# Performance work log

Hardware: AMD Instinct MI355X
Metric: run time of the kernel (lower is better)

## Reference

```python
import math
import jax, jax.numpy as jnp
import numpy as np


def _precompute_psi(nlat_in, nlon_in, nlat_out, K, theta_cutoff):
    """Faithful numpy port of _precompute_convolution_tensor (equiangular grids).
    Returns COO indices (k, t, lat_in, lon_in) and float values of the sparse
    filter tensor psi of logical shape [K, nlat_out, nlat_in*nlon_in]."""
    lats_in = np.linspace(0.0, np.pi, nlat_in)
    lats_out = np.linspace(0.0, np.pi, nlat_out)
    phis = np.linspace(-np.pi, np.pi, nlon_in)
    d_theta = theta_cutoff / K
    theta_i = np.arange(K) * d_theta  # (K,)
    ks, ts, las, los, vs = [], [], [], [], []
    alpha = -lats_in[:, None]          # (nlat_in, 1)
    beta = phis[None, :]               # (1, nlon_in)
    for t in range(nlat_out):
        gamma = lats_out[t]
        z = np.cos(alpha) * np.cos(gamma) - np.cos(beta) * np.sin(alpha) * np.sin(gamma)
        theta = np.arccos(np.clip(z, -1.0, 1.0))   # (nlat_in, nlon_in)
        diff = np.abs(theta[None, :, :] - theta_i[:, None, None])  # (K, nlat_in, nlon_in)
        mask = (diff < d_theta) & (theta[None, :, :] < theta_cutoff)
        k_idx, la_idx, lo_idx = np.nonzero(mask)
        v = 1.0 - diff[k_idx, la_idx, lo_idx] / d_theta  # triangle (hat) weights
        ks.append(k_idx); ts.append(np.full_like(k_idx, t)); las.append(la_idx); los.append(lo_idx); vs.append(v)
    return (np.concatenate(ks).astype(np.int32),
            np.concatenate(ts).astype(np.int32),
            np.concatenate(las).astype(np.int32),
            np.concatenate(los).astype(np.int32),
            np.concatenate(vs).astype(np.float32))


def setup_inputs() -> dict:
    B, C = 4, 32
    nlat_in, nlon_in = 361, 720
    nlat_out, nlon_out = 361, 720
    K = 3
    theta_cutoff = 0.01 * math.pi  # default used at the precompute call site
    k, t, la, lo, v = _precompute_psi(nlat_in, nlon_in, nlat_out, K, theta_cutoff)
    key = jax.random.key(0)
    x = jax.random.normal(key, (B, C, nlat_in, nlon_in), dtype=jnp.float32)
    return {
        "x": x,
        "psi_vals": jnp.asarray(v),
        "psi_k": jnp.asarray(k),
        "psi_t": jnp.asarray(t),
        "psi_lat": jnp.asarray(la),
        "psi_lon": jnp.asarray(lo),
        "kernel_size": K,
        "nlat_out": nlat_out,
        "nlon_out": nlon_out,
    }


def reference(x, psi_vals, psi_k, psi_t, psi_lat, psi_lon, kernel_size, nlat_out, nlon_out):
    B, C, nlat_in, nlon_in = x.shape
    BC = B * C
    scale = nlon_in // nlon_out  # = 1 here
    # (nlat_in, nlon_in, BC) layout, matching x.reshape(B*C,...).permute(1,2,0)
    xr = x.reshape(BC, nlat_in, nlon_in).transpose(1, 2, 0)
    seg = psi_k * nlat_out + psi_t           # row id in the (K*nlat_out) output
    num_seg = kernel_size * nlat_out

    def step(_, p):
        # torch.roll(x, scale, dims=lon) applied (p+1) times before the bmm:
        # rolled[lat, lon] = x[lat, (lon - (p+1)*scale) % nlon]
        lon_idx = (psi_lon - (p + 1) * scale) % nlon_in
        g = xr[psi_lat, lon_idx]             # (nnz, BC) irregular gather
        out_p = jax.ops.segment_sum(psi_vals[:, None] * g, seg, num_segments=num_seg)
        return None, out_p                   # (K*nlat_out, BC)

    _, outs = jax.lax.scan(step, None, jnp.arange(nlon_out))  # (nlon_out, K*nlat_out, BC)
    outs = outs.reshape(nlon_out, kernel_size, nlat_out, BC)
    # permute(3,1,2,0) then split BC -> (B, C)
    return outs.transpose(3, 1, 2, 0).reshape(B, C, kernel_size, nlat_out, nlon_out)
```

## Files before the change

kernel.cpp:

```cpp
#include <hip/hip_runtime.h>
#include <math.h>


#define NLAT 361
#define NLON 720
#define KK 3
#define PTILE 48
#define NPX 15
#define NT 384
#define PD 56
#define SWN 832
#define TOTCAP (720*1024)

typedef __attribute__((ext_vector_type(8))) short bf16x8;
typedef __attribute__((ext_vector_type(4))) float f32x4;
typedef __attribute__((ext_vector_type(4))) unsigned int u32x4;

#define D_PI 3.14159265358979311599796346854418516159057617187500
#define STEP_LAT (D_PI / 360.0)
#define STEP_PHI ((2.0 * D_PI) / 719.0)
#define CUTOFF (0.01 * D_PI)
#define DTH (CUTOFF / 3.0)

__device__ __forceinline__ void gll16(const void* g, void* l) {
    __builtin_amdgcn_global_load_lds(
        (const __attribute__((address_space(1))) void*)g,
        (__attribute__((address_space(3))) void*)l, 16, 0, 0);
}
__device__ __forceinline__ void gll4(const void* g, void* l) {
    __builtin_amdgcn_global_load_lds(
        (const __attribute__((address_space(1))) void*)g,
        (__attribute__((address_space(3))) void*)l, 4, 0, 0);
}

__device__ inline unsigned int bf16pair_rne(float lo, float hi) {
    unsigned int a = __builtin_bit_cast(unsigned int, lo);
    unsigned int b = __builtin_bit_cast(unsigned int, hi);
    a = a + 0x7fffu + ((a >> 16) & 1u);
    b = b + 0x7fffu + ((b >> 16) & 1u);
    return (a >> 16) | (b & 0xffff0000u);
}

__global__ __launch_bounds__(512) void bounds_kernel(int4* __restrict__ params,
                                                     float2* __restrict__ pAB,
                                                     unsigned long long* __restrict__ actd) {
    __shared__ int part[512];
    int tid = threadIdx.x;
    int rmins[9], Ws[9], bl8s[9];
    float As[9], Bs[9];
    int wsum = 0;
    if (tid < NLAT) {
        int t = tid;
        double g = (t == 360) ? D_PI : (double)t * STEP_LAT;
        double cg = cos(g), sg = sin(g);
        const double coscut = cos(CUTOFF);
#pragma unroll
        for (int d = 0; d < 9; ++d) {
            int la = t + d - 4;
            int rmin = 0, W = 0;
            double A = 0.0, Bc = 0.0;
            if (la >= 0 && la <= 360) {
                double lad = (la == 360) ? D_PI : (double)la * STEP_LAT;
                A = cos(lad) * cg;
                Bc = sin(lad) * sg;
                if (Bc < 1e-14) {
                    if (A > coscut) { rmin = 0; W = 720; }
                } else {
                    double C = (coscut - A) / Bc;
                    if (C <= -1.0) { rmin = 0; W = 720; }
                    else if (C < 1.0) {
                        double bmax = acos(C);
                        int r0 = (int)floor((D_PI - bmax) / STEP_PHI) + 1;
                        int r1 = (int)ceil((D_PI + bmax) / STEP_PHI) - 1;
                        if (r0 < 0) r0 = 0;
                        if (r1 > 719) r1 = 719;
                        rmin = r0; W = r1 - r0 + 1;
                        if (W < 0) W = 0;
                    }
                }
            }
            rmins[d] = rmin; Ws[d] = W;
            As[d] = (float)A; Bs[d] = (float)Bc;
            int b8 = 0;
            if (W > 0) {
                b8 = (W + 111) & ~7;
                if (b8 > SWN) b8 = SWN;
            }
            bl8s[d] = b8;
            wsum += b8;
        }
    }
    part[tid] = wsum;
    __syncthreads();
    for (int dd = 1; dd < 512; dd <<= 1) {
        int v = part[tid];
        int w2 = (tid >= dd) ? part[tid - dd] : 0;
        __syncthreads();
        part[tid] = v + w2;
        __syncthreads();
    }
    int base = part[tid] - wsum;
    if (tid < NLAT) {
        unsigned long long pk = 0;
        int nact = 0;
#pragma unroll
        for (int d = 0; d < 9; ++d) {
            int off = base;
            base += bl8s[d];
            if (Ws[d] > 0 && off + bl8s[d] <= TOTCAP) {
                params[tid * 9 + d] = make_int4(rmins[d], Ws[d], off, bl8s[d]);
                pAB[tid * 9 + d] = make_float2(As[d], Bs[d]);
                pk |= ((unsigned long long)d) << (4 + 4 * nact);
                nact++;
            } else {
                params[tid * 9 + d] = make_int4(0, 0, 0, 0);
            }
        }
        pk |= (unsigned long long)nact;
        actd[tid] = pk;
    }
}

__global__ __launch_bounds__(128) void fill_w_kernel(const int4* __restrict__ params,
                                                     const float2* __restrict__ pAB,
                                                     unsigned int* __restrict__ wtab) {
    int row = blockIdx.x;
    int4 pr = params[row];
    int W = pr.y;
    if (W <= 0) return;
    int rmin = pr.x, off = pr.z, bl8 = pr.w;
    float2 ab = pAB[row];
    float A = ab.x, Bc = ab.y;
    const float invd = (float)(1.0 / DTH);
    for (int idx = threadIdx.x; idx < bl8; idx += 128) {
        int j = idx - PD;
        float f1 = 1.0e9f, f2 = 1.0e9f;
        if (j >= 0 && j < W) {
            int lo = rmin + j;
            float beta = (lo == 719) ? (float)D_PI : (float)((double)lo * STEP_PHI - D_PI);
            float z = fminf(1.f, fmaxf(-1.f, fmaf(Bc, cosf(beta), A)));
            f1 = acosf(z) * invd;
        }
        if (j + 1 >= 0 && j + 1 < W) {
            int lo = rmin + j + 1;
            float beta = (lo == 719) ? (float)D_PI : (float)((double)lo * STEP_PHI - D_PI);
            float z = fminf(1.f, fmaxf(-1.f, fmaf(Bc, cosf(beta), A)));
            f2 = acosf(z) * invd;
        }
        float w0a = fmaxf(0.f, 1.f - f1);
        float w1a = fmaxf(0.f, 1.f - fabsf(f1 - 1.f));
        float w2a = fmaxf(0.f, 1.f - fabsf(f1 - 2.f));
        float w0b = fmaxf(0.f, 1.f - f2);
        float w1b = fmaxf(0.f, 1.f - fabsf(f2 - 1.f));
        float w2b = fmaxf(0.f, 1.f - fabsf(f2 - 2.f));
        wtab[0 * TOTCAP + off + idx] = bf16pair_rne(w0a, w0b);
        wtab[1 * TOTCAP + off + idx] = bf16pair_rne(w1a, w1b);
        wtab[2 * TOTCAP + off + idx] = bf16pair_rne(w2a, w2b);
    }
}

__global__ void cvt_x_kernel(const float* __restrict__ x, unsigned int* __restrict__ xb,
                             int n8) {
    for (int i = blockIdx.x * 256 + threadIdx.x; i < n8; i += gridDim.x * 256) {
        f32x4 a = *(const f32x4*)(x + (size_t)i * 8);
        f32x4 b = *(const f32x4*)(x + (size_t)i * 8 + 4);
        u32x4 q;
        q.x = bf16pair_rne(a.x, a.y);
        q.y = bf16pair_rne(a.z, a.w);
        q.z = bf16pair_rne(b.x, b.y);
        q.w = bf16pair_rne(b.z, b.w);
        *(u32x4*)(xb + (size_t)i * 4) = q;
    }
}

template <int USEBF16>
__global__ __launch_bounds__(NT, 4) void dconv_mfma_kernel(
    const float* __restrict__ x, const unsigned short* __restrict__ xb,
    const int4* __restrict__ params, const unsigned long long* __restrict__ actd,
    const unsigned int* __restrict__ wtab, float* __restrict__ out) {
    __shared__ __attribute__((aligned(16))) unsigned char sB[2][128 * 128];
    __shared__ unsigned int sWi[2][KK * SWN];

    int bid = blockIdx.x;
    int r = bid & 7;
    int rest = bid >> 3;
    int px = rest % NPX;
    int q = rest / NPX;
    int yp = 8 * q + r;
    if (yp > 360) return;
    int t = (yp & 1) ? (360 - (yp >> 1)) : (yp >> 1);
    int p0 = px * PTILE;
    int tid = threadIdx.x;
    int lane = tid & 63;
    int w = tid >> 6;
    int psub = w >> 1;
    int bc0w = (w & 1) * 64;
    int l15 = lane & 15;
    int l4 = lane >> 4;

    f32x4 acc[4][KK];
#pragma unroll
    for (int n = 0; n < 4; ++n)
#pragma unroll
        for (int k = 0; k < KK; ++k) acc[n][k] = (f32x4){0.f, 0.f, 0.f, 0.f};

    unsigned long long pk = actd[t];
    int nact = (int)(pk & 15ull);

    int c = 0, iact = 0;
    int la = 0, W = 0, off = 0, bl8 = 0, mbase = 0, shift = 0;
    int nK = 0, nC = 1, ks_lo = 0, ks_hi = -1;

    auto LOADP = [&](int dd) {
        la = t + dd - 4;
        int4 pr = params[t * 9 + dd];
        int rmin = pr.x;
        W = pr.y; off = pr.z; bl8 = pr.w;
        int ms0 = rmin - 48 - p0;
        shift = (ms0 + 720) & 7;
        nK = (W + 47 + shift + 31) >> 5;
        nC = (nK + 1) >> 1;
        mbase = (((ms0 - shift) % 720) + 720) % 720;
        int s_off = psub * 16 + 9 - shift;
        int kl = (9 - s_off + 31) >> 5;
        ks_lo = kl < 0 ? 0 : kl;
        int kh = (55 + W - s_off) >> 5;
        ks_hi = kh > nK - 1 ? nK - 1 : kh;
    };

    auto ISSUE = [&](int cc, bool rowstart, int pbuf, int rbuf) {
#pragma unroll
        for (int pass = 0; pass < 3; ++pass) {
            int slot = pass * NT + tid;
            if (slot < 1024) {
                int bc = slot >> 3;
                int g = slot & 7;
                int gs = g ^ (bc & 7);
                int mg = mbase + cc * 64 + gs * 8;
                mg -= (mg >= 720) ? 720 : 0;
                mg -= (mg >= 720) ? 720 : 0;
                mg -= (mg >= 720) ? 720 : 0;
                if (USEBF16) {
                    gll16(xb + ((size_t)bc * NLAT + la) * NLON + mg,
                          &sB[pbuf][slot * 16]);
                } else {
                    const float* src = x + ((size_t)bc * NLAT + la) * NLON + mg;
                    f32x4 a = *(const f32x4*)(src);
                    f32x4 b = *(const f32x4*)(src + 4);
                    u32x4 qq;
                    qq.x = bf16pair_rne(a.x, a.y);
                    qq.y = bf16pair_rne(a.z, a.w);
                    qq.z = bf16pair_rne(b.x, b.y);
                    qq.w = bf16pair_rne(b.z, b.w);
                    *(u32x4*)(&sB[pbuf][slot * 16]) = qq;
                }
            }
        }
        if (rowstart) {
#pragma unroll
            for (int pass = 0; pass < 3; ++pass) {
                int idx = pass * NT + tid;
                if (idx < bl8) {
                    if (USEBF16) {
                        gll4(wtab + 0 * TOTCAP + off + idx, &sWi[rbuf][0 * SWN + idx]);
                        gll4(wtab + 1 * TOTCAP + off + idx, &sWi[rbuf][1 * SWN + idx]);
                        gll4(wtab + 2 * TOTCAP + off + idx, &sWi[rbuf][2 * SWN + idx]);
                    } else {
                        sWi[rbuf][0 * SWN + idx] = wtab[0 * TOTCAP + off + idx];
                        sWi[rbuf][1 * SWN + idx] = wtab[1 * TOTCAP + off + idx];
                        sWi[rbuf][2 * SWN + idx] = wtab[2 * TOTCAP + off + idx];
                    }
                }
            }
        }
    };

    LOADP((int)((pk >> 4) & 15ull));
    ISSUE(0, true, 0, 0);
    int pb = 0, rw = 0;

    while (true) {
        int shiftS = shift;
        int c2 = c * 2;
        int kloS = ks_lo > c2 ? ks_lo : c2;
        int khiS = ks_hi < c2 + 1 ? ks_hi : c2 + 1;
        int pbC = pb, rwC = rw;
        bool done = false, nrow = false;
        if (c + 1 < nC) {
            c = c + 1;
        } else if (iact + 1 < nact) {
            iact++;
            c = 0;
            LOADP((int)((pk >> (4 + 4 * iact)) & 15ull));
            nrow = true;
        } else {
            done = true;
        }
        if (USEBF16) asm volatile("s_waitcnt vmcnt(0)" ::: "memory");
        __syncthreads();
        if (!done) {
            pb ^= 1;
            if (nrow) rw ^= 1;
            ISSUE(c, nrow, pb, rw);
        }
        int soffS = psub * 16 + 9 - shiftS;
        for (int ks = kloS; ks <= khiS; ++ks) {
            int ksl = ks - c2;
            int s = ks * 32 + l4 * 8 + soffS + l15;
            bf16x8 af[KK];
#pragma unroll
            for (int k = 0; k < KK; ++k) {
                const unsigned int* wp = &sWi[rwC][k * SWN + s];
                u32x4 qf;
                qf.x = wp[0];
                qf.y = wp[2];
                qf.z = wp[4];
                qf.w = wp[6];
                af[k] = __builtin_bit_cast(bf16x8, qf);
            }
            int colbase = ksl * 64 + l4 * 16;
#pragma unroll
            for (int n = 0; n < 4; ++n) {
                int brow = bc0w + n * 16 + l15;
                int colb = colbase ^ ((brow & 7) << 4);
                bf16x8 bfv = *(const bf16x8*)(&sB[pbC][brow * 128 + colb]);
                acc[n][0] = __builtin_amdgcn_mfma_f32_16x16x32_bf16(af[0], bfv, acc[n][0], 0, 0, 0);
                acc[n][1] = __builtin_amdgcn_mfma_f32_16x16x32_bf16(af[1], bfv, acc[n][1], 0, 0, 0);
                acc[n][2] = __builtin_amdgcn_mfma_f32_16x16x32_bf16(af[2], bfv, acc[n][2], 0, 0, 0);
            }
        }
        if (done) break;
    }

    int p = p0 + psub * 16 + l4 * 4;
#pragma unroll
    for (int n = 0; n < 4; ++n) {
        int bc = bc0w + n * 16 + l15;
#pragma unroll
        for (int k = 0; k < KK; ++k) {
            float* o = out + (((size_t)bc * KK + k) * NLAT + t) * NLON + p;
            *(f32x4*)o = acc[n][k];
        }
    }
}

extern "C" void kernel_launch(void* const* d_in, const int* in_sizes, int n_in,
                              void* d_out, int out_size, void* d_ws, size_t ws_size,
                              hipStream_t stream) {
    const float* x = (const float*)d_in[0];
    float* out = (float*)d_out;

    char* ws = (char*)d_ws;
    int4* params = (int4*)(ws + 0);
    float2* pAB = (float2*)(ws + 53248);
    unsigned long long* actd = (unsigned long long*)(ws + 81920);
    unsigned int* wtab = (unsigned int*)(ws + 90112);
    size_t xb_off = (90112 + (size_t)3 * TOTCAP * 4 + 4095) & ~(size_t)4095;
    size_t xb_bytes = (size_t)128 * NLAT * NLON * 2;
    int use_bf16 = (ws_size >= xb_off + xb_bytes) ? 1 : 0;
    unsigned short* xb = (unsigned short*)(ws + xb_off);

    bounds_kernel<<<1, 512, 0, stream>>>(params, pAB, actd);
    fill_w_kernel<<<NLAT * 9, 128, 0, stream>>>(params, pAB, wtab);

    dim3 grid(8 * NPX * 46, 1, 1);
    if (use_bf16) {
        int n8 = 128 * NLAT * NLON / 8;
        cvt_x_kernel<<<2048, 256, 0, stream>>>(x, (unsigned int*)xb, n8);
        dconv_mfma_kernel<1><<<grid, NT, 0, stream>>>(x, xb, params, actd, wtab, out);
    } else {
        dconv_mfma_kernel<0><<<grid, NT, 0, stream>>>(x, xb, params, actd, wtab, out);
    }
}
```

Before: 292.4 us.

## Read filter weights directly from global memory instead of staging in LDS

The weight table is re-laid out so the three kernel-size weights for each position sit next to each other (interleaved by 3). The LDS staging buffer for weights and its per-row async loads are removed. Each wave now loads its A-fragments straight from global or L2 into registers before issuing the next B tile, and the inner k-step loop is unrolled into two fixed halves. This cuts LDS usage, which may raise occupancy, and removes the per-row weight copy. The cost is scattered, non-vectorised global loads that sit on the critical path after the barrier.

```diff
diff --git a/kernel.cpp b/kernel.cpp
--- a/kernel.cpp
+++ b/kernel.cpp
@@ -26,11 +26,6 @@
     __builtin_amdgcn_global_load_lds(
         (const __attribute__((address_space(1))) void*)g,
         (__attribute__((address_space(3))) void*)l, 16, 0, 0);
-}
-__device__ __forceinline__ void gll4(const void* g, void* l) {
-    __builtin_amdgcn_global_load_lds(
-        (const __attribute__((address_space(1))) void*)g,
-        (__attribute__((address_space(3))) void*)l, 4, 0, 0);
 }
 
 __device__ inline unsigned int bf16pair_rne(float lo, float hi) {
@@ -153,9 +148,10 @@
         float w0b = fmaxf(0.f, 1.f - f2);
         float w1b = fmaxf(0.f, 1.f - fabsf(f2 - 1.f));
         float w2b = fmaxf(0.f, 1.f - fabsf(f2 - 2.f));
-        wtab[0 * TOTCAP + off + idx] = bf16pair_rne(w0a, w0b);
-        wtab[1 * TOTCAP + off + idx] = bf16pair_rne(w1a, w1b);
-        wtab[2 * TOTCAP + off + idx] = bf16pair_rne(w2a, w2b);
+        size_t e = (size_t)(off + idx) * 3;
+        wtab[e + 0] = bf16pair_rne(w0a, w0b);
+        wtab[e + 1] = bf16pair_rne(w1a, w1b);
+        wtab[e + 2] = bf16pair_rne(w2a, w2b);
     }
 }
 
@@ -179,7 +175,6 @@
     const int4* __restrict__ params, const unsigned long long* __restrict__ actd,
     const unsigned int* __restrict__ wtab, float* __restrict__ out) {
     __shared__ __attribute__((aligned(16))) unsigned char sB[2][128 * 128];
-    __shared__ unsigned int sWi[2][KK * SWN];
 
     int bid = blockIdx.x;
     int r = bid & 7;
@@ -208,14 +203,14 @@
     int nact = (int)(pk & 15ull);
 
     int c = 0, iact = 0;
-    int la = 0, W = 0, off = 0, bl8 = 0, mbase = 0, shift = 0;
+    int la = 0, W = 0, off = 0, mbase = 0, shift = 0;
     int nK = 0, nC = 1, ks_lo = 0, ks_hi = -1;
 
     auto LOADP = [&](int dd) {
         la = t + dd - 4;
         int4 pr = params[t * 9 + dd];
         int rmin = pr.x;
-        W = pr.y; off = pr.z; bl8 = pr.w;
+        W = pr.y; off = pr.z;
         int ms0 = rmin - 48 - p0;
         shift = (ms0 + 720) & 7;
         nK = (W + 47 + shift + 31) >> 5;
@@ -228,7 +223,7 @@
         ks_hi = kh > nK - 1 ? nK - 1 : kh;
     };
 
-    auto ISSUE = [&](int cc, bool rowstart, int pbuf, int rbuf) {
+    auto ISSUE = [&](int cc, int pbuf) {
 #pragma unroll
         for (int pass = 0; pass < 3; ++pass) {
             int slot = pass * NT + tid;
@@ -256,69 +251,63 @@
                 }
             }
         }
-        if (rowstart) {
-#pragma unroll
-            for (int pass = 0; pass < 3; ++pass) {
-                int idx = pass * NT + tid;
-                if (idx < bl8) {
-                    if (USEBF16) {
-                        gll4(wtab + 0 * TOTCAP + off + idx, &sWi[rbuf][0 * SWN + idx]);
-                        gll4(wtab + 1 * TOTCAP + off + idx, &sWi[rbuf][1 * SWN + idx]);
-                        gll4(wtab + 2 * TOTCAP + off + idx, &sWi[rbuf][2 * SWN + idx]);
-                    } else {
-                        sWi[rbuf][0 * SWN + idx] = wtab[0 * TOTCAP + off + idx];
-                        sWi[rbuf][1 * SWN + idx] = wtab[1 * TOTCAP + off + idx];
-                        sWi[rbuf][2 * SWN + idx] = wtab[2 * TOTCAP + off + idx];
-                    }
-                }
-            }
-        }
     };
 
     LOADP((int)((pk >> 4) & 15ull));
-    ISSUE(0, true, 0, 0);
-    int pb = 0, rw = 0;
+    ISSUE(0, 0);
+    int pb = 0;
 
     while (true) {
-        int shiftS = shift;
         int c2 = c * 2;
-        int kloS = ks_lo > c2 ? ks_lo : c2;
-        int khiS = ks_hi < c2 + 1 ? ks_hi : c2 + 1;
-        int pbC = pb, rwC = rw;
-        bool done = false, nrow = false;
+        bool do0 = (c2 >= ks_lo) && (c2 <= ks_hi);
+        bool do1 = (c2 + 1 >= ks_lo) && (c2 + 1 <= ks_hi);
+        int soffS = psub * 16 + 9 - shift;
+        int offS = off;
+        int pbC = pb;
+        bool done = false;
         if (c + 1 < nC) {
             c = c + 1;
         } else if (iact + 1 < nact) {
             iact++;
             c = 0;
             LOADP((int)((pk >> (4 + 4 * iact)) & 15ull));
-            nrow = true;
         } else {
             done = true;
         }
         if (USEBF16) asm volatile("s_waitcnt vmcnt(0)" ::: "memory");
         __syncthreads();
+        unsigned int A0[KK][4], A1[KK][4];
+        if (do0) {
+            int s0 = c2 * 32 + l4 * 8 + soffS + l15;
+            const unsigned int* bp = wtab + (size_t)(offS + s0) * 3;
+#pragma unroll
+            for (int e = 0; e < 4; ++e)
+#pragma unroll
+                for (int k = 0; k < KK; ++k)
+                    A0[k][e] = bp[e * 6 + k];
+        }
+        if (do1) {
+            int s1 = (c2 + 1) * 32 + l4 * 8 + soffS + l15;
+            const unsigned int* bp = wtab + (size_t)(offS + s1) * 3;
+#pragma unroll
+            for (int e = 0; e < 4; ++e)
+#pragma unroll
+                for (int k = 0; k < KK; ++k)
+                    A1[k][e] = bp[e * 6 + k];
+        }
         if (!done) {
             pb ^= 1;
-            if (nrow) rw ^= 1;
-            ISSUE(c, nrow, pb, rw);
-        }
-        int soffS = psub * 16 + 9 - shiftS;
-        for (int ks = kloS; ks <= khiS; ++ks) {
-            int ksl = ks - c2;
-            int s = ks * 32 + l4 * 8 + soffS + l15;
+            ISSUE(c, pb);
+        }
+        if (do0) {
             bf16x8 af[KK];
 #pragma unroll
             for (int k = 0; k < KK; ++k) {
-                const unsigned int* wp = &sWi[rwC][k * SWN + s];
                 u32x4 qf;
-                qf.x = wp[0];
-                qf.y = wp[2];
-                qf.z = wp[4];
-                qf.w = wp[6];
+                qf.x = A0[k][0]; qf.y = A0[k][1]; qf.z = A0[k][2]; qf.w = A0[k][3];
                 af[k] = __builtin_bit_cast(bf16x8, qf);
             }
-            int colbase = ksl * 64 + l4 * 16;
+            int colbase = l4 * 16;
 #pragma unroll
             for (int n = 0; n < 4; ++n) {
                 int brow = bc0w + n * 16 + l15;
@@ -329,6 +318,25 @@
                 acc[n][2] = __builtin_amdgcn_mfma_f32_16x16x32_bf16(af[2], bfv, acc[n][2], 0, 0, 0);
             }
         }
+        if (do1) {
+            bf16x8 af[KK];
+#pragma unroll
+            for (int k = 0; k < KK; ++k) {
+                u32x4 qf;
+                qf.x = A1[k][0]; qf.y = A1[k][1]; qf.z = A1[k][2]; qf.w = A1[k][3];
+                af[k] = __builtin_bit_cast(bf16x8, qf);
+            }
+            int colbase = 64 + l4 * 16;
+#pragma unroll
+            for (int n = 0; n < 4; ++n) {
+                int brow = bc0w + n * 16 + l15;
+                int colb = colbase ^ ((brow & 7) << 4);
+                bf16x8 bfv = *(const bf16x8*)(&sB[pbC][brow * 128 + colb]);
+                acc[n][0] = __builtin_amdgcn_mfma_f32_16x16x32_bf16(af[0], bfv, acc[n][0], 0, 0, 0);
+                acc[n][1] = __builtin_amdgcn_mfma_f32_16x16x32_bf16(af[1], bfv, acc[n][1], 0, 0, 0);
+                acc[n][2] = __builtin_amdgcn_mfma_f32_16x16x32_bf16(af[2], bfv, acc[n][2], 0, 0, 0);
+            }
+        }
         if (done) break;
     }
 
@@ -355,7 +363,7 @@
     float2* pAB = (float2*)(ws + 53248);
     unsigned long long* actd = (unsigned long long*)(ws + 81920);
     unsigned int* wtab = (unsigned int*)(ws + 90112);
-    size_t xb_off = (90112 + (size_t)3 * TOTCAP * 4 + 4095) & ~(size_t)4095;
+    size_t xb_off = (90112 + (size_t)TOTCAP * 12 + 4095) & ~(size_t)4095;
     size_t xb_bytes = (size_t)128 * NLAT * NLON * 2;
     int use_bf16 = (ws_size >= xb_off + xb_bytes) ? 1 : 0;
     unsigned short* xb = (unsigned short*)(ws + xb_off);
```

Result: slower. 308.2 us (+5.4%).

## Double chunk width to 128 columns and stream weight slices per chunk

Applied to the files above, without the earlier changes.

Each pipeline stage now stages 128 longitude columns per bc row instead of 64, so there are half as many barrier-synchronised chunks. Filter weights are no longer loaded once per active latitude row into a large table. Instead a small 192-entry slice per plane is double-buffered alongside each B chunk. Shared memory per block grows to about 68 KB and launch bounds drop to 3 blocks per SM, trading occupancy for fewer syncs and a simpler weight-load path. The inner k-step loop is unrolled by 4 with guards.

```diff
diff --git a/kernel.cpp b/kernel.cpp
--- a/kernel.cpp
+++ b/kernel.cpp
@@ -10,7 +10,9 @@
 #define NT 384
 #define PD 56
 #define SWN 832
+#define SWNP 192
 #define TOTCAP (720*1024)
+#define BUFB (128*256)
 
 typedef __attribute__((ext_vector_type(8))) short bf16x8;
 typedef __attribute__((ext_vector_type(4))) float f32x4;
@@ -174,19 +176,19 @@
 }
 
 template <int USEBF16>
-__global__ __launch_bounds__(NT, 4) void dconv_mfma_kernel(
+__global__ __launch_bounds__(NT, 3) void dconv_mfma_kernel(
     const float* __restrict__ x, const unsigned short* __restrict__ xb,
     const int4* __restrict__ params, const unsigned long long* __restrict__ actd,
     const unsigned int* __restrict__ wtab, float* __restrict__ out) {
-    __shared__ __attribute__((aligned(16))) unsigned char sB[2][128 * 128];
-    __shared__ unsigned int sWi[2][KK * SWN];
+    __shared__ __attribute__((aligned(16))) unsigned char sB[2][BUFB];
+    __shared__ __attribute__((aligned(16))) unsigned int sWi[2][3 * SWNP];
 
     int bid = blockIdx.x;
     int r = bid & 7;
     int rest = bid >> 3;
     int px = rest % NPX;
-    int q = rest / NPX;
-    int yp = 8 * q + r;
+    int qg = rest / NPX;
+    int yp = 8 * qg + r;
     if (yp > 360) return;
     int t = (yp & 1) ? (360 - (yp >> 1)) : (yp >> 1);
     int p0 = px * PTILE;
@@ -208,18 +210,18 @@
     int nact = (int)(pk & 15ull);
 
     int c = 0, iact = 0;
-    int la = 0, W = 0, off = 0, bl8 = 0, mbase = 0, shift = 0;
+    int la = 0, W = 0, off = 0, mbase = 0, shift = 0;
     int nK = 0, nC = 1, ks_lo = 0, ks_hi = -1;
 
     auto LOADP = [&](int dd) {
         la = t + dd - 4;
         int4 pr = params[t * 9 + dd];
         int rmin = pr.x;
-        W = pr.y; off = pr.z; bl8 = pr.w;
+        W = pr.y; off = pr.z;
         int ms0 = rmin - 48 - p0;
         shift = (ms0 + 720) & 7;
         nK = (W + 47 + shift + 31) >> 5;
-        nC = (nK + 1) >> 1;
+        nC = (nK + 3) >> 2;
         mbase = (((ms0 - shift) % 720) + 720) % 720;
         int s_off = psub * 16 + 9 - shift;
         int kl = (9 - s_off + 31) >> 5;
@@ -228,15 +230,15 @@
         ks_hi = kh > nK - 1 ? nK - 1 : kh;
     };
 
-    auto ISSUE = [&](int cc, bool rowstart, int pbuf, int rbuf) {
-#pragma unroll
-        for (int pass = 0; pass < 3; ++pass) {
+    auto ISSUE = [&](int cc, int pbuf) {
+#pragma unroll
+        for (int pass = 0; pass < 6; ++pass) {
             int slot = pass * NT + tid;
-            if (slot < 1024) {
-                int bc = slot >> 3;
-                int g = slot & 7;
-                int gs = g ^ (bc & 7);
-                int mg = mbase + cc * 64 + gs * 8;
+            if (slot < 2048) {
+                int bc = slot >> 4;
+                int g = slot & 15;
+                int gs = (g & 8) | ((g ^ (bc & 7)) & 7);
+                int mg = mbase + cc * 128 + gs * 8;
                 mg -= (mg >= 720) ? 720 : 0;
                 mg -= (mg >= 720) ? 720 : 0;
                 mg -= (mg >= 720) ? 720 : 0;
@@ -256,43 +258,40 @@
                 }
             }
         }
-        if (rowstart) {
-#pragma unroll
-            for (int pass = 0; pass < 3; ++pass) {
-                int idx = pass * NT + tid;
-                if (idx < bl8) {
-                    if (USEBF16) {
-                        gll4(wtab + 0 * TOTCAP + off + idx, &sWi[rbuf][0 * SWN + idx]);
-                        gll4(wtab + 1 * TOTCAP + off + idx, &sWi[rbuf][1 * SWN + idx]);
-                        gll4(wtab + 2 * TOTCAP + off + idx, &sWi[rbuf][2 * SWN + idx]);
-                    } else {
-                        sWi[rbuf][0 * SWN + idx] = wtab[0 * TOTCAP + off + idx];
-                        sWi[rbuf][1 * SWN + idx] = wtab[1 * TOTCAP + off + idx];
-                        sWi[rbuf][2 * SWN + idx] = wtab[2 * TOTCAP + off + idx];
-                    }
+#pragma unroll
+        for (int pass = 0; pass < 2; ++pass) {
+            int slot = pass * NT + tid;
+            if (slot < 3 * SWNP) {
+                int plane = slot / SWNP;
+                int e = slot - plane * SWNP;
+                int gidx = off + cc * 128 + e;
+                gidx = (gidx > TOTCAP - 1) ? (TOTCAP - 1) : gidx;
+                if (USEBF16) {
+                    gll4(wtab + (size_t)plane * TOTCAP + gidx, &sWi[pbuf][slot]);
+                } else {
+                    sWi[pbuf][slot] = wtab[(size_t)plane * TOTCAP + gidx];
                 }
             }
         }
     };
 
     LOADP((int)((pk >> 4) & 15ull));
-    ISSUE(0, true, 0, 0);
-    int pb = 0, rw = 0;
+    ISSUE(0, 0);
+    int pb = 0;
 
     while (true) {
-        int shiftS = shift;
-        int c2 = c * 2;
-        int kloS = ks_lo > c2 ? ks_lo : c2;
-        int khiS = ks_hi < c2 + 1 ? ks_hi : c2 + 1;
-        int pbC = pb, rwC = rw;
-        bool done = false, nrow = false;
+        int c4 = c * 4;
+        int s_off = psub * 16 + 9 - shift;
+        int kl = ks_lo > c4 ? ks_lo : c4;
+        int kh = ks_hi < c4 + 3 ? ks_hi : c4 + 3;
+        int pbC = pb;
+        bool done = false;
         if (c + 1 < nC) {
             c = c + 1;
         } else if (iact + 1 < nact) {
             iact++;
             c = 0;
             LOADP((int)((pk >> (4 + 4 * iact)) & 15ull));
-            nrow = true;
         } else {
             done = true;
         }
@@ -300,17 +299,17 @@
         __syncthreads();
         if (!done) {
             pb ^= 1;
-            if (nrow) rw ^= 1;
-            ISSUE(c, nrow, pb, rw);
-        }
-        int soffS = psub * 16 + 9 - shiftS;
-        for (int ks = kloS; ks <= khiS; ++ks) {
-            int ksl = ks - c2;
-            int s = ks * 32 + l4 * 8 + soffS + l15;
+            ISSUE(c, pb);
+        }
+#pragma unroll
+        for (int ksl = 0; ksl < 4; ++ksl) {
+            int ks = c4 + ksl;
+            if (ks < kl || ks > kh) continue;
+            int lidx = ksl * 32 + l4 * 8 + s_off + l15;
             bf16x8 af[KK];
 #pragma unroll
             for (int k = 0; k < KK; ++k) {
-                const unsigned int* wp = &sWi[rwC][k * SWN + s];
+                const unsigned int* wp = &sWi[pbC][k * SWNP + lidx];
                 u32x4 qf;
                 qf.x = wp[0];
                 qf.y = wp[2];
@@ -323,7 +322,7 @@
             for (int n = 0; n < 4; ++n) {
                 int brow = bc0w + n * 16 + l15;
                 int colb = colbase ^ ((brow & 7) << 4);
-                bf16x8 bfv = *(const bf16x8*)(&sB[pbC][brow * 128 + colb]);
+                bf16x8 bfv = *(const bf16x8*)(&sB[pbC][brow * 256 + colb]);
                 acc[n][0] = __builtin_amdgcn_mfma_f32_16x16x32_bf16(af[0], bfv, acc[n][0], 0, 0, 0);
                 acc[n][1] = __builtin_amdgcn_mfma_f32_16x16x32_bf16(af[1], bfv, acc[n][1], 0, 0, 0);
                 acc[n][2] = __builtin_amdgcn_mfma_f32_16x16x32_bf16(af[2], bfv, acc[n][2], 0, 0, 0);
```

Result: slower. 372.9 us (+27.5%).
